# Optimization experiments

Hardware: AMD Instinct MI355X
Metric: run time of the kernel (lower is better)

## Reference

```python
import jax, jax.numpy as jnp
import numpy as np
import math

B, W, D_IN, H = 64, 512, 300, 512

def setup_inputs() -> dict:
    key = jax.random.key(0)
    ks = jax.random.split(key, 8)
    s = 1.0 / math.sqrt(D_IN)
    return {
        "char_vectors": jax.random.normal(ks[0], (B, W, D_IN), jnp.float32),
        "word_vectors": jax.random.normal(ks[1], (B, W, D_IN), jnp.float32),
        "Wk": jax.random.uniform(ks[2], (D_IN, H), jnp.float32, -s, s),
        "bk": jnp.zeros((H,), jnp.float32),
        "Wq": jax.random.uniform(ks[3], (D_IN, H), jnp.float32, -s, s),
        "bq": jnp.zeros((H,), jnp.float32),
        "Wv": jax.random.uniform(ks[4], (D_IN, H), jnp.float32, -s, s),
        "bv": jnp.zeros((H,), jnp.float32),
    }

def reference(char_vectors, word_vectors, Wk, bk, Wq, bq, Wv, bv):
    # Stack word/char reps per word -> [B, W, 2, H]
    def proj(Wm, bm):
        return jnp.stack([word_vectors @ Wm + bm, char_vectors @ Wm + bm], axis=2)
    K = proj(Wk, bk)
    Q = proj(Wq, bq)
    V = proj(Wv, bv)
    temp = jnp.sqrt(jnp.asarray(H, jnp.float32))
    # tiny 2x2 attention per word, fully batched (dropout off = eval mode)
    attn = jnp.einsum("bwqh,bwkh->bwqk", Q, K) / temp
    attn = jax.nn.softmax(attn, axis=-1)
    out = jnp.einsum("bwqk,bwkh->bwqh", attn, V)  # [B, W, 2, H]
    return out.reshape(B, W, 2 * H)
```

## Files before the change

### kernel.cpp

```cpp
#include <hip/hip_runtime.h>

#define D 300
#define HDIM 512
#define ROWS 256
#define WPB 128
#define NKS 20
#define NCH 24
#define CH_BYTES 40960
#define CH_ELEMS 20480
#define REG_BYTES 20480
#define SEGW 5

typedef __attribute__((ext_vector_type(16))) float f32x16;
typedef __attribute__((ext_vector_type(4))) float f32x4;
typedef __attribute__((ext_vector_type(8))) short bf16x8;

__device__ inline unsigned short f2bf(float f) {
  unsigned int u = __float_as_uint(f);
  unsigned int r = (u + 0x7fffu + ((u >> 16) & 1u)) >> 16;
  return (unsigned short)r;
}

__device__ inline void gload_lds16(const void* g, void* l) {
  __builtin_amdgcn_global_load_lds(
      (const __attribute__((address_space(1))) unsigned int*)g,
      (__attribute__((address_space(3))) unsigned int*)l, 16, 0, 0);
}

__global__ __launch_bounds__(512) void prep_weights(
    const float* __restrict__ Wq, const float* __restrict__ Wk,
    const float* __restrict__ Wv, unsigned short* __restrict__ wt) {
  int idx = blockIdx.x * 512 + threadIdx.x;
  if (idx >= NCH * CH_ELEMS) return;
  int c = idx / CH_ELEMS, r = idx - c * CH_ELEMS;
  int reg = r / 10240, r2 = r - reg * 10240;
  int ks = r2 >> 9, r3 = r2 & 511;
  int kh = r3 >> 8, r4 = r3 & 255;
  int col = r4 >> 3, e = r4 & 7;
  int k = ks * 16 + kh * 8 + e;
  const float* M; int gcol;
  if (c < 16) { M = reg ? Wk : Wq; gcol = c * 32 + col; }
  else        { M = Wv; gcol = (c - 16) * 64 + reg * 32 + col; }
  float v = (k < D) ? M[k * HDIM + gcol] : 0.0f;
  wt[idx] = f2bf(v);
}

__global__ __launch_bounds__(512) void fused_attn(
    const float* __restrict__ charv, const float* __restrict__ wordv,
    const unsigned short* __restrict__ wt,
    const float* __restrict__ bk, const float* __restrict__ bq,
    const float* __restrict__ bv, float* __restrict__ out) {
  extern __shared__ char lds[];
  float* biasL = (float*)(lds + 3 * CH_BYTES);
  float* sS    = biasL + 1536;
  float* sAt   = sS;

  const int tid  = threadIdx.x;
  const int wid  = tid >> 6;
  const int lane = tid & 63;
  const int lo5  = lane & 31;
  const int hi   = lane >> 5;

  auto stage = [&](int t) {
    const char* src = (const char*)wt + (long)t * CH_BYTES + wid * (SEGW * 1024) + lane * 16;
    char* dst = lds + (t % 3) * CH_BYTES + wid * (SEGW * 1024);
#pragma unroll
    for (int j = 0; j < SEGW; ++j)
      gload_lds16(src + j * 1024, dst + j * 1024);
  };

  for (int i = tid; i < 1536; i += 512) {
    float v = (i < 512) ? bq[i] : ((i < 1024) ? bk[i - 512] : bv[i - 1024]);
    biasL[i] = v;
  }
  bf16x8 a[NKS];
  {
    int row = blockIdx.x * ROWS + wid * 32 + lo5;
    const float* rp = ((row & 1) ? charv : wordv) + (row >> 1) * D;
#pragma unroll
    for (int ks = 0; ks < NKS; ++ks) {
      int k0 = ks * 16 + hi * 8;
      float4 lo = {0.f, 0.f, 0.f, 0.f}, hif = {0.f, 0.f, 0.f, 0.f};
      if (k0 + 8 <= D) {
        lo  = *(const float4*)(rp + k0);
        hif = *(const float4*)(rp + k0 + 4);
      } else if (k0 < D) {
        lo  = *(const float4*)(rp + k0);
      }
      bf16x8 v;
      v[0] = (short)f2bf(lo.x);  v[1] = (short)f2bf(lo.y);
      v[2] = (short)f2bf(lo.z);  v[3] = (short)f2bf(lo.w);
      v[4] = (short)f2bf(hif.x); v[5] = (short)f2bf(hif.y);
      v[6] = (short)f2bf(hif.z); v[7] = (short)f2bf(hif.w);
      a[ks] = v;
    }
  }
  stage(0);
  stage(1);

  float p[32];
#pragma unroll
  for (int t = 0; t < 32; ++t) p[t] = 0.f;

  for (int t = 0; t < 16; ++t) {
    asm volatile("s_waitcnt vmcnt(5)" ::: "memory");
    asm volatile("s_waitcnt lgkmcnt(0)" ::: "memory");
    __builtin_amdgcn_s_barrier();
    stage(t + 2);
    const char* base = lds + (t % 3) * CH_BYTES + hi * 512 + lo5 * 16;
    float bqv = biasL[t * 32 + lo5];
    float bkv = biasL[512 + t * 32 + lo5];
    f32x16 accQ, accK;
#pragma unroll
    for (int r = 0; r < 16; ++r) { accQ[r] = bqv; accK[r] = bkv; }
#pragma unroll
    for (int ks = 0; ks < NKS; ++ks) {
      bf16x8 qb = *(const bf16x8*)(base + ks * 1024);
      bf16x8 kb = *(const bf16x8*)(base + REG_BYTES + ks * 1024);
      accQ = __builtin_amdgcn_mfma_f32_32x32x16_bf16(a[ks], qb, accQ, 0, 0, 0);
      accK = __builtin_amdgcn_mfma_f32_32x32x16_bf16(a[ks], kb, accK, 0, 0, 0);
    }
#pragma unroll
    for (int tt = 0; tt < 8; ++tt)
#pragma unroll
      for (int i = 0; i < 2; ++i)
#pragma unroll
        for (int j = 0; j < 2; ++j)
          p[tt * 4 + i * 2 + j] += accQ[2 * tt + i] * accK[2 * tt + j];
  }

#pragma unroll
  for (int t = 0; t < 32; ++t) {
    float v = p[t];
    v += __shfl_xor(v, 1);
    v += __shfl_xor(v, 2);
    v += __shfl_xor(v, 4);
    v += __shfl_xor(v, 8);
    v += __shfl_xor(v, 16);
    p[t] = v;
  }
  if (lo5 == 0) {
#pragma unroll
    for (int tt = 0; tt < 8; ++tt) {
      int w = wid * 16 + (tt >> 1) * 4 + (tt & 1) + hi * 2;
#pragma unroll
      for (int q = 0; q < 4; ++q) sS[w * 4 + q] = p[tt * 4 + q];
    }
  }
  asm volatile("s_waitcnt lgkmcnt(0)" ::: "memory");
  __builtin_amdgcn_s_barrier();
  if (tid < 128) {
    const float sc = 0.044194173824159216f;
    float s[4];
#pragma unroll
    for (int t = 0; t < 4; ++t) s[t] = sS[tid * 4 + t] * sc;
#pragma unroll
    for (int i = 0; i < 2; ++i) {
      float m  = fmaxf(s[i * 2], s[i * 2 + 1]);
      float e0 = expf(s[i * 2] - m), e1 = expf(s[i * 2 + 1] - m);
      float inv = 1.0f / (e0 + e1);
      sAt[tid * 4 + i * 2]     = e0 * inv;
      sAt[tid * 4 + i * 2 + 1] = e1 * inv;
    }
  }
  asm volatile("s_waitcnt lgkmcnt(0)" ::: "memory");
  __builtin_amdgcn_s_barrier();

  f32x4 at[8];
#pragma unroll
  for (int tt = 0; tt < 8; ++tt) {
    int w = wid * 16 + (tt >> 1) * 4 + (tt & 1) + hi * 2;
    at[tt] = *(const f32x4*)(sAt + w * 4);
  }

  for (int t = 16; t < NCH; ++t) {
    if (t == 16) asm volatile("s_waitcnt vmcnt(5)" ::: "memory");
    else         asm volatile("s_waitcnt vmcnt(37)" ::: "memory");
    asm volatile("s_waitcnt lgkmcnt(0)" ::: "memory");
    __builtin_amdgcn_s_barrier();
    if (t + 2 < NCH) stage(t + 2);
    const char* base = lds + (t % 3) * CH_BYTES + hi * 512 + lo5 * 16;
    const int g = t - 16;
#pragma unroll
    for (int ct = 0; ct < 2; ++ct) {
      float bvv = biasL[1024 + g * 64 + ct * 32 + lo5];
      f32x16 accV;
#pragma unroll
      for (int r = 0; r < 16; ++r) accV[r] = bvv;
#pragma unroll
      for (int ks = 0; ks < NKS; ++ks) {
        bf16x8 vb = *(const bf16x8*)(base + ct * REG_BYTES + ks * 1024);
        accV = __builtin_amdgcn_mfma_f32_32x32x16_bf16(a[ks], vb, accV, 0, 0, 0);
      }
      int h = g * 64 + ct * 32 + lo5;
#pragma unroll
      for (int tt = 0; tt < 8; ++tt) {
        int w = wid * 16 + (tt >> 1) * 4 + (tt & 1) + hi * 2;
        long gw = (long)(blockIdx.x * WPB + w);
        float v0 = accV[2 * tt], v1 = accV[2 * tt + 1];
        out[gw * 1024 + h]       = at[tt][0] * v0 + at[tt][1] * v1;
        out[gw * 1024 + 512 + h] = at[tt][2] * v0 + at[tt][3] * v1;
      }
    }
  }
}

extern "C" void kernel_launch(void* const* d_in, const int* in_sizes, int n_in,
                              void* d_out, int out_size, void* d_ws, size_t ws_size,
                              hipStream_t stream) {
  const float* charv = (const float*)d_in[0];
  const float* wordv = (const float*)d_in[1];
  const float* Wk = (const float*)d_in[2];
  const float* bk = (const float*)d_in[3];
  const float* Wq = (const float*)d_in[4];
  const float* bq = (const float*)d_in[5];
  const float* Wv = (const float*)d_in[6];
  const float* bv = (const float*)d_in[7];
  float* out = (float*)d_out;
  unsigned short* wt = (unsigned short*)d_ws;

  prep_weights<<<(NCH * CH_ELEMS + 511) / 512, 512, 0, stream>>>(Wq, Wk, Wv, wt);

  const int lds_bytes = 3 * CH_BYTES + 1536 * 4 + 512 * 4;
  fused_attn<<<65536 / ROWS, 512, lds_bytes, stream>>>(charv, wordv, wt, bk, bq, bv, out);
}
```

Before: 87.47 us.

## Halve block tile to 128 rows and split weight chunks per projection

Shrinks each block from 512 to 256 threads and from 256 to 128 rows, which doubles the grid. Weight chunks are halved so the Q, K and V panels each stream as their own LDS chunk. The Q/K loop now has two barrier-separated stages per column group, and the V epilogue handles one 32-column tile per chunk. The aim is a smaller LDS footprint so more blocks can fit per CU, giving better occupancy and load balance. The cost is twice the total weight staging traffic and more barriers.

```diff
diff --git a/kernel.cpp b/kernel.cpp
--- a/kernel.cpp
+++ b/kernel.cpp
@@ -2,13 +2,12 @@
 
 #define D 300
 #define HDIM 512
-#define ROWS 256
-#define WPB 128
+#define ROWS 128
+#define WPB 64
 #define NKS 20
-#define NCH 24
-#define CH_BYTES 40960
-#define CH_ELEMS 20480
-#define REG_BYTES 20480
+#define NCH 48
+#define CH_BYTES 20480
+#define CH_ELEMS 10240
 #define SEGW 5
 
 typedef __attribute__((ext_vector_type(16))) float f32x16;
@@ -32,20 +31,19 @@
     const float* __restrict__ Wv, unsigned short* __restrict__ wt) {
   int idx = blockIdx.x * 512 + threadIdx.x;
   if (idx >= NCH * CH_ELEMS) return;
-  int c = idx / CH_ELEMS, r = idx - c * CH_ELEMS;
-  int reg = r / 10240, r2 = r - reg * 10240;
+  int c = idx / CH_ELEMS, r2 = idx - c * CH_ELEMS;
   int ks = r2 >> 9, r3 = r2 & 511;
   int kh = r3 >> 8, r4 = r3 & 255;
   int col = r4 >> 3, e = r4 & 7;
   int k = ks * 16 + kh * 8 + e;
   const float* M; int gcol;
-  if (c < 16) { M = reg ? Wk : Wq; gcol = c * 32 + col; }
-  else        { M = Wv; gcol = (c - 16) * 64 + reg * 32 + col; }
+  if (c < 32) { M = (c & 1) ? Wk : Wq; gcol = (c >> 1) * 32 + col; }
+  else        { M = Wv; gcol = (c - 32) * 32 + col; }
   float v = (k < D) ? M[k * HDIM + gcol] : 0.0f;
   wt[idx] = f2bf(v);
 }
 
-__global__ __launch_bounds__(512) void fused_attn(
+__global__ __launch_bounds__(256) void fused_attn(
     const float* __restrict__ charv, const float* __restrict__ wordv,
     const unsigned short* __restrict__ wt,
     const float* __restrict__ bk, const float* __restrict__ bq,
@@ -69,7 +67,7 @@
       gload_lds16(src + j * 1024, dst + j * 1024);
   };
 
-  for (int i = tid; i < 1536; i += 512) {
+  for (int i = tid; i < 1536; i += 256) {
     float v = (i < 512) ? bq[i] : ((i < 1024) ? bk[i - 512] : bv[i - 1024]);
     biasL[i] = v;
   }
@@ -102,31 +100,47 @@
 #pragma unroll
   for (int t = 0; t < 32; ++t) p[t] = 0.f;
 
-  for (int t = 0; t < 16; ++t) {
+  f32x16 accQ;
+
+  for (int g = 0; g < 16; ++g) {
     asm volatile("s_waitcnt vmcnt(5)" ::: "memory");
     asm volatile("s_waitcnt lgkmcnt(0)" ::: "memory");
     __builtin_amdgcn_s_barrier();
-    stage(t + 2);
-    const char* base = lds + (t % 3) * CH_BYTES + hi * 512 + lo5 * 16;
-    float bqv = biasL[t * 32 + lo5];
-    float bkv = biasL[512 + t * 32 + lo5];
-    f32x16 accQ, accK;
-#pragma unroll
-    for (int r = 0; r < 16; ++r) { accQ[r] = bqv; accK[r] = bkv; }
-#pragma unroll
-    for (int ks = 0; ks < NKS; ++ks) {
-      bf16x8 qb = *(const bf16x8*)(base + ks * 1024);
-      bf16x8 kb = *(const bf16x8*)(base + REG_BYTES + ks * 1024);
-      accQ = __builtin_amdgcn_mfma_f32_32x32x16_bf16(a[ks], qb, accQ, 0, 0, 0);
-      accK = __builtin_amdgcn_mfma_f32_32x32x16_bf16(a[ks], kb, accK, 0, 0, 0);
-    }
-#pragma unroll
-    for (int tt = 0; tt < 8; ++tt)
-#pragma unroll
-      for (int i = 0; i < 2; ++i)
-#pragma unroll
-        for (int j = 0; j < 2; ++j)
-          p[tt * 4 + i * 2 + j] += accQ[2 * tt + i] * accK[2 * tt + j];
+    stage(2 * g + 2);
+    {
+      const char* base = lds + ((2 * g) % 3) * CH_BYTES + hi * 512 + lo5 * 16;
+      float bqv = biasL[g * 32 + lo5];
+#pragma unroll
+      for (int r = 0; r < 16; ++r) accQ[r] = bqv;
+#pragma unroll
+      for (int ks = 0; ks < NKS; ++ks) {
+        bf16x8 qb = *(const bf16x8*)(base + ks * 1024);
+        accQ = __builtin_amdgcn_mfma_f32_32x32x16_bf16(a[ks], qb, accQ, 0, 0, 0);
+      }
+    }
+    asm volatile("s_waitcnt vmcnt(5)" ::: "memory");
+    asm volatile("s_waitcnt lgkmcnt(0)" ::: "memory");
+    __builtin_amdgcn_s_barrier();
+    stage(2 * g + 3);
+    {
+      const char* base = lds + ((2 * g + 1) % 3) * CH_BYTES + hi * 512 + lo5 * 16;
+      float bkv = biasL[512 + g * 32 + lo5];
+      f32x16 accK;
+#pragma unroll
+      for (int r = 0; r < 16; ++r) accK[r] = bkv;
+#pragma unroll
+      for (int ks = 0; ks < NKS; ++ks) {
+        bf16x8 kb = *(const bf16x8*)(base + ks * 1024);
+        accK = __builtin_amdgcn_mfma_f32_32x32x16_bf16(a[ks], kb, accK, 0, 0, 0);
+      }
+#pragma unroll
+      for (int tt = 0; tt < 8; ++tt)
+#pragma unroll
+        for (int i = 0; i < 2; ++i)
+#pragma unroll
+          for (int j = 0; j < 2; ++j)
+            p[tt * 4 + i * 2 + j] += accQ[2 * tt + i] * accK[2 * tt + j];
+    }
   }
 
 #pragma unroll
@@ -149,7 +163,7 @@
   }
   asm volatile("s_waitcnt lgkmcnt(0)" ::: "memory");
   __builtin_amdgcn_s_barrier();
-  if (tid < 128) {
+  if (tid < 64) {
     const float sc = 0.044194173824159216f;
     float s[4];
 #pragma unroll
@@ -173,34 +187,31 @@
     at[tt] = *(const f32x4*)(sAt + w * 4);
   }
 
-  for (int t = 16; t < NCH; ++t) {
-    if (t == 16) asm volatile("s_waitcnt vmcnt(5)" ::: "memory");
-    else         asm volatile("s_waitcnt vmcnt(37)" ::: "memory");
+  for (int t = 32; t < NCH; ++t) {
+    if (t == 32) asm volatile("s_waitcnt vmcnt(5)" ::: "memory");
+    else         asm volatile("s_waitcnt vmcnt(21)" ::: "memory");
     asm volatile("s_waitcnt lgkmcnt(0)" ::: "memory");
     __builtin_amdgcn_s_barrier();
     if (t + 2 < NCH) stage(t + 2);
     const char* base = lds + (t % 3) * CH_BYTES + hi * 512 + lo5 * 16;
-    const int g = t - 16;
-#pragma unroll
-    for (int ct = 0; ct < 2; ++ct) {
-      float bvv = biasL[1024 + g * 64 + ct * 32 + lo5];
-      f32x16 accV;
-#pragma unroll
-      for (int r = 0; r < 16; ++r) accV[r] = bvv;
-#pragma unroll
-      for (int ks = 0; ks < NKS; ++ks) {
-        bf16x8 vb = *(const bf16x8*)(base + ct * REG_BYTES + ks * 1024);
-        accV = __builtin_amdgcn_mfma_f32_32x32x16_bf16(a[ks], vb, accV, 0, 0, 0);
-      }
-      int h = g * 64 + ct * 32 + lo5;
-#pragma unroll
-      for (int tt = 0; tt < 8; ++tt) {
-        int w = wid * 16 + (tt >> 1) * 4 + (tt & 1) + hi * 2;
-        long gw = (long)(blockIdx.x * WPB + w);
-        float v0 = accV[2 * tt], v1 = accV[2 * tt + 1];
-        out[gw * 1024 + h]       = at[tt][0] * v0 + at[tt][1] * v1;
-        out[gw * 1024 + 512 + h] = at[tt][2] * v0 + at[tt][3] * v1;
-      }
+    const int g = t - 32;
+    float bvv = biasL[1024 + g * 32 + lo5];
+    f32x16 accV;
+#pragma unroll
+    for (int r = 0; r < 16; ++r) accV[r] = bvv;
+#pragma unroll
+    for (int ks = 0; ks < NKS; ++ks) {
+      bf16x8 vb = *(const bf16x8*)(base + ks * 1024);
+      accV = __builtin_amdgcn_mfma_f32_32x32x16_bf16(a[ks], vb, accV, 0, 0, 0);
+    }
+    int h = g * 32 + lo5;
+#pragma unroll
+    for (int tt = 0; tt < 8; ++tt) {
+      int w = wid * 16 + (tt >> 1) * 4 + (tt & 1) + hi * 2;
+      long gw = (long)(blockIdx.x * WPB + w);
+      float v0 = accV[2 * tt], v1 = accV[2 * tt + 1];
+      out[gw * 1024 + h]       = at[tt][0] * v0 + at[tt][1] * v1;
+      out[gw * 1024 + 512 + h] = at[tt][2] * v0 + at[tt][3] * v1;
     }
   }
 }
@@ -222,5 +233,5 @@
   prep_weights<<<(NCH * CH_ELEMS + 511) / 512, 512, 0, stream>>>(Wq, Wk, Wv, wt);
 
   const int lds_bytes = 3 * CH_BYTES + 1536 * 4 + 512 * 4;
-  fused_attn<<<65536 / ROWS, 512, lds_bytes, stream>>>(charv, wordv, wt, bk, bq, bv, out);
-}
+  fused_attn<<<65536 / ROWS, 256, lds_bytes, stream>>>(charv, wordv, wt, bk, bq, bv, out);
+}
```

Result: slower. 89.41 us (+2.2%).

## Fold biases into padded K row, issue weight staging earlier, raise MFMA priority

Applied to the files above, without the earlier changes.

Folds the biases into the bf16 weight buffer as an extra row at k=300 and sets the matching activation element to 1.0, so the MFMA adds the bias and the LDS bias table and its loads go away. Weight staging for the first two chunks now starts before the activation loads, so the global-to-LDS copies overlap the row fetch. It also raises wave priority with s_setprio around the MFMA loops. The bias now goes through bf16 rounding, which adds a small precision loss; with zero biases this has no effect.

```diff
diff --git a/kernel.cpp b/kernel.cpp
--- a/kernel.cpp
+++ b/kernel.cpp
@@ -29,7 +29,9 @@
 
 __global__ __launch_bounds__(512) void prep_weights(
     const float* __restrict__ Wq, const float* __restrict__ Wk,
-    const float* __restrict__ Wv, unsigned short* __restrict__ wt) {
+    const float* __restrict__ Wv, const float* __restrict__ bq,
+    const float* __restrict__ bk, const float* __restrict__ bv,
+    unsigned short* __restrict__ wt) {
   int idx = blockIdx.x * 512 + threadIdx.x;
   if (idx >= NCH * CH_ELEMS) return;
   int c = idx / CH_ELEMS, r = idx - c * CH_ELEMS;
@@ -38,22 +40,22 @@
   int kh = r3 >> 8, r4 = r3 & 255;
   int col = r4 >> 3, e = r4 & 7;
   int k = ks * 16 + kh * 8 + e;
-  const float* M; int gcol;
-  if (c < 16) { M = reg ? Wk : Wq; gcol = c * 32 + col; }
-  else        { M = Wv; gcol = (c - 16) * 64 + reg * 32 + col; }
-  float v = (k < D) ? M[k * HDIM + gcol] : 0.0f;
+  const float* M; const float* B; int gcol;
+  if (c < 16) {
+    M = reg ? Wk : Wq; B = reg ? bk : bq; gcol = c * 32 + col;
+  } else {
+    M = Wv; B = bv; gcol = (c - 16) * 64 + reg * 32 + col;
+  }
+  float v = (k < D) ? M[k * HDIM + gcol] : ((k == D) ? B[gcol] : 0.0f);
   wt[idx] = f2bf(v);
 }
 
 __global__ __launch_bounds__(512) void fused_attn(
     const float* __restrict__ charv, const float* __restrict__ wordv,
-    const unsigned short* __restrict__ wt,
-    const float* __restrict__ bk, const float* __restrict__ bq,
-    const float* __restrict__ bv, float* __restrict__ out) {
+    const unsigned short* __restrict__ wt, float* __restrict__ out) {
   extern __shared__ char lds[];
-  float* biasL = (float*)(lds + 3 * CH_BYTES);
-  float* sS    = biasL + 1536;
-  float* sAt   = sS;
+  float* sS  = (float*)(lds + 3 * CH_BYTES);
+  float* sAt = sS;
 
   const int tid  = threadIdx.x;
   const int wid  = tid >> 6;
@@ -69,10 +71,9 @@
       gload_lds16(src + j * 1024, dst + j * 1024);
   };
 
-  for (int i = tid; i < 1536; i += 512) {
-    float v = (i < 512) ? bq[i] : ((i < 1024) ? bk[i - 512] : bv[i - 1024]);
-    biasL[i] = v;
-  }
+  stage(0);
+  stage(1);
+
   bf16x8 a[NKS];
   {
     int row = blockIdx.x * ROWS + wid * 32 + lo5;
@@ -92,11 +93,10 @@
       v[2] = (short)f2bf(lo.z);  v[3] = (short)f2bf(lo.w);
       v[4] = (short)f2bf(hif.x); v[5] = (short)f2bf(hif.y);
       v[6] = (short)f2bf(hif.z); v[7] = (short)f2bf(hif.w);
+      if (ks == 18 && hi == 1) v[4] = (short)0x3F80;
       a[ks] = v;
     }
   }
-  stage(0);
-  stage(1);
 
   float p[32];
 #pragma unroll
@@ -108,11 +108,10 @@
     __builtin_amdgcn_s_barrier();
     stage(t + 2);
     const char* base = lds + (t % 3) * CH_BYTES + hi * 512 + lo5 * 16;
-    float bqv = biasL[t * 32 + lo5];
-    float bkv = biasL[512 + t * 32 + lo5];
     f32x16 accQ, accK;
 #pragma unroll
-    for (int r = 0; r < 16; ++r) { accQ[r] = bqv; accK[r] = bkv; }
+    for (int r = 0; r < 16; ++r) { accQ[r] = 0.f; accK[r] = 0.f; }
+    __builtin_amdgcn_s_setprio(1);
 #pragma unroll
     for (int ks = 0; ks < NKS; ++ks) {
       bf16x8 qb = *(const bf16x8*)(base + ks * 1024);
@@ -120,6 +119,7 @@
       accQ = __builtin_amdgcn_mfma_f32_32x32x16_bf16(a[ks], qb, accQ, 0, 0, 0);
       accK = __builtin_amdgcn_mfma_f32_32x32x16_bf16(a[ks], kb, accK, 0, 0, 0);
     }
+    __builtin_amdgcn_s_setprio(0);
 #pragma unroll
     for (int tt = 0; tt < 8; ++tt)
 #pragma unroll
@@ -183,15 +183,16 @@
     const int g = t - 16;
 #pragma unroll
     for (int ct = 0; ct < 2; ++ct) {
-      float bvv = biasL[1024 + g * 64 + ct * 32 + lo5];
       f32x16 accV;
 #pragma unroll
-      for (int r = 0; r < 16; ++r) accV[r] = bvv;
+      for (int r = 0; r < 16; ++r) accV[r] = 0.f;
+      __builtin_amdgcn_s_setprio(1);
 #pragma unroll
       for (int ks = 0; ks < NKS; ++ks) {
         bf16x8 vb = *(const bf16x8*)(base + ct * REG_BYTES + ks * 1024);
         accV = __builtin_amdgcn_mfma_f32_32x32x16_bf16(a[ks], vb, accV, 0, 0, 0);
       }
+      __builtin_amdgcn_s_setprio(0);
       int h = g * 64 + ct * 32 + lo5;
 #pragma unroll
       for (int tt = 0; tt < 8; ++tt) {
@@ -219,8 +220,9 @@
   float* out = (float*)d_out;
   unsigned short* wt = (unsigned short*)d_ws;
 
-  prep_weights<<<(NCH * CH_ELEMS + 511) / 512, 512, 0, stream>>>(Wq, Wk, Wv, wt);
-
-  const int lds_bytes = 3 * CH_BYTES + 1536 * 4 + 512 * 4;
-  fused_attn<<<65536 / ROWS, 512, lds_bytes, stream>>>(charv, wordv, wt, bk, bq, bv, out);
-}
+  prep_weights<<<(NCH * CH_ELEMS + 511) / 512, 512, 0, stream>>>(
+      Wq, Wk, Wv, bq, bk, bv, wt);
+
+  const int lds_bytes = 3 * CH_BYTES + 512 * 4;
+  fused_attn<<<65536 / ROWS, 512, lds_bytes, stream>>>(charv, wordv, wt, out);
+}
```

New measurement: 87.96 us. About the same (+0.6%).
